# Optimization experiments

Hardware: AMD Instinct MI355X
Metric: run time of the kernel (lower is better)

The kernel has to match this reference:

```python
import jax, jax.numpy as jnp
import numpy as np

B, T, C, D = 8, 4096, 1024, 128  # batch, seq (=block_size), dim_embd, head_features

def setup_inputs() -> dict:
    key = jax.random.key(0)
    k1, k2, k3, k4 = jax.random.split(key, 4)
    s = 0.02
    return {
        "x": jax.random.normal(k1, (B, T, C), dtype=jnp.float32),
        "wq": jax.random.normal(k2, (C, D), dtype=jnp.float32) * s,
        "wk": jax.random.normal(k3, (C, D), dtype=jnp.float32) * s,
        "wv": jax.random.normal(k4, (C, D), dtype=jnp.float32) * s,
    }

def reference(x, wq, wk, wv):
    # q,k,v: [B,T,D]
    q = jnp.einsum('btc,cd->btd', x, wq)
    k = jnp.einsum('btc,cd->btd', x, wk)
    v = jnp.einsum('btc,cd->btd', x, wv)
    scale = k.shape[-1] ** -0.5
    wei = jnp.einsum('bqd,bkd->bqk', q, k) * scale  # [B,T,T]
    causal = jnp.tril(jnp.ones((T, T), dtype=bool))
    wei = jnp.where(causal, wei, -jnp.inf)
    attn = jax.nn.softmax(wei, axis=-1)  # dropout p=0.0 -> identity
    out = jnp.einsum('bqk,bkd->bqd', attn, v)  # [B,T,D]
    return out
```

## Files before the change

### kernel.cpp

```cpp
#include <hip/hip_runtime.h>

#define TT 4096
#define CC 1024
#define DD 128

typedef __attribute__((ext_vector_type(8))) short s16x8;
typedef __attribute__((ext_vector_type(4))) short s16x4;
typedef __attribute__((ext_vector_type(8))) __bf16 bf16x8;
typedef __attribute__((ext_vector_type(4))) float f32x4;

__device__ __forceinline__ short f2bf(float f) {
    union { float f; unsigned u; } v; v.f = f;
    unsigned r = v.u + 0x7fffu + ((v.u >> 16) & 1u);
    return (short)(r >> 16);
}

__device__ __forceinline__ unsigned cvt_pk(float lo, float hi) {
    unsigned r;
    asm("v_cvt_pk_bf16_f32 %0, %1, %2" : "=v"(r) : "v"(lo), "v"(hi));
    return r;
}

__device__ __forceinline__ f32x4 mfma16(s16x8 a, s16x8 b, f32x4 c) {
    return __builtin_amdgcn_mfma_f32_16x16x32_bf16(
        __builtin_bit_cast(bf16x8, a), __builtin_bit_cast(bf16x8, b), c, 0, 0, 0);
}

__device__ __forceinline__ void gload_lds16(const short* g, short* l) {
    __builtin_amdgcn_global_load_lds(
        (const __attribute__((address_space(1))) void*)g,
        (__attribute__((address_space(3))) void*)l, 16, 0, 0);
}

__global__ void wt_kernel(const float* __restrict__ wq, const float* __restrict__ wk,
                          const float* __restrict__ wv, short* __restrict__ wT) {
    int idx = blockIdx.x * 256 + threadIdx.x;
    int d = idx & 127;
    int c = (idx >> 7) & 1023;
    int wsel = idx >> 17;
    const float* w = (wsel == 0) ? wq : (wsel == 1) ? wk : wv;
    float v = w[(size_t)c * DD + d];
    if (wsel == 0) v *= 0.08838834764831845f;
    wT[(size_t)wsel * DD * CC + (size_t)d * CC + c] = f2bf(v);
}

__global__ __launch_bounds__(512)
void qkv_kernel(const float* __restrict__ x, const short* __restrict__ wT,
                short* __restrict__ qo, short* __restrict__ ko, short* __restrict__ vTo) {
    __shared__ short lw[2][384 * 64];
    const int mt = blockIdx.x;
    const int tid = threadIdx.x, lane = tid & 63, wid = tid >> 6;
    const int l15 = lane & 15, g = lane >> 4;
    const int wm = wid >> 1, wn = wid & 1;
    const int arow = mt * 128 + wm * 32 + l15;
    const float* xr0 = x + (size_t)arow * CC + g * 8;
    const float* xr1 = xr0 + (size_t)16 * CC;

    const f32x4 fz = {0.f, 0.f, 0.f, 0.f};
    f32x4 acc[2][12];
#pragma unroll
    for (int mr = 0; mr < 2; mr++)
#pragma unroll
        for (int nr = 0; nr < 12; nr++) acc[mr][nr] = fz;

    const int swr = wid * 48;
    const short* wsrc = wT + (size_t)(swr + (lane >> 3)) * CC + (lane & 7) * 8;

    float4 pa[2][2][2];
#define LOADA(kc) do { \
    _Pragma("unroll") for (int mr_ = 0; mr_ < 2; mr_++) \
    _Pragma("unroll") for (int ks_ = 0; ks_ < 2; ks_++) { \
        const float* p_ = (mr_ ? xr1 : xr0) + (kc) * 64 + ks_ * 32; \
        pa[mr_][ks_][0] = *(const float4*)p_; \
        pa[mr_][ks_][1] = *(const float4*)(p_ + 4); } \
} while (0)
#define STAGEW(kc, buf) do { \
    _Pragma("unroll") for (int j_ = 0; j_ < 6; j_++) \
        gload_lds16(wsrc + (size_t)(j_ * 8) * CC + (kc) * 64, &lw[buf][(swr + j_ * 8) * 64]); \
} while (0)

    LOADA(0);
    STAGEW(0, 0);
    asm volatile("s_waitcnt vmcnt(0)" ::: "memory");
    __builtin_amdgcn_s_barrier();
    int cur = 0;

    for (int kc = 0; kc < 16; kc++) {
        s16x8 af[2][2];
#pragma unroll
        for (int mr = 0; mr < 2; mr++)
#pragma unroll
            for (int ks = 0; ks < 2; ks++) {
                union { unsigned u[4]; s16x8 v; } cv;
                cv.u[0] = cvt_pk(pa[mr][ks][0].x, pa[mr][ks][0].y);
                cv.u[1] = cvt_pk(pa[mr][ks][0].z, pa[mr][ks][0].w);
                cv.u[2] = cvt_pk(pa[mr][ks][1].x, pa[mr][ks][1].y);
                cv.u[3] = cvt_pk(pa[mr][ks][1].z, pa[mr][ks][1].w);
                af[mr][ks] = cv.v;
            }
        if (kc < 15) { LOADA(kc + 1); STAGEW(kc + 1, cur ^ 1); }
        __builtin_amdgcn_s_setprio(1);
#pragma unroll
        for (int ks = 0; ks < 2; ks++)
#pragma unroll
            for (int nr = 0; nr < 12; nr++) {
                const s16x8 bfg = *(const s16x8*)
                    &lw[cur][(wn * 192 + nr * 16 + l15) * 64 + ks * 32 + g * 8];
                acc[0][nr] = mfma16(af[0][ks], bfg, acc[0][nr]);
                acc[1][nr] = mfma16(af[1][ks], bfg, acc[1][nr]);
            }
        __builtin_amdgcn_s_setprio(0);
        asm volatile("s_waitcnt vmcnt(0) lgkmcnt(0)" ::: "memory");
        __builtin_amdgcn_s_barrier();
        cur ^= 1;
    }

    const int bidx = mt >> 5;
    const int tb = (mt & 31) * 128 + wm * 32;
#pragma unroll
    for (int mr = 0; mr < 2; mr++)
#pragma unroll
        for (int nr = 0; nr < 12; nr++) {
            const int n = wn * 192 + nr * 16 + l15;
            if (n < 256) {
                short* dst; int d;
                if (n < 128) { dst = qo; d = n; } else { dst = ko; d = n - 128; }
#pragma unroll
                for (int i = 0; i < 4; i++) {
                    int t = tb + mr * 16 + g * 4 + i;
                    dst[((size_t)bidx * TT + t) * DD + d] = f2bf(acc[mr][nr][i]);
                }
            } else {
                const int d = n - 256;
                const int t = tb + mr * 16 + g * 4;
                uint2 u;
                u.x = cvt_pk(acc[mr][nr][0], acc[mr][nr][1]);
                u.y = cvt_pk(acc[mr][nr][2], acc[mr][nr][3]);
                *(uint2*)(vTo + ((size_t)bidx * DD + d) * TT + t) = u;
            }
        }
}

__device__ __forceinline__ void attn_stage(const short* kT, const short* vT, int kv0,
                                           short* lkb, short* lvb, int wid, int lane) {
#pragma unroll
    for (int j = 0; j < 4; j++) {
        int rbk = wid * 16 + j * 4;
        int rk = rbk + (lane >> 4);
        int ck = (lane & 15) ^ (rk & 7);
        gload_lds16(kT + (size_t)(kv0 + rk) * DD + ck * 8, lkb + rbk * 128);
        int rbv = wid * 32 + j * 8;
        int dv = rbv + (lane >> 3);
        int cv = (lane & 7) ^ (dv & 7);
        gload_lds16(vT + (size_t)dv * TT + kv0 + cv * 8, lvb + rbv * 64);
    }
}

__global__ __launch_bounds__(256)
void attn_kernel(const short* __restrict__ qb, const short* __restrict__ kb,
                 const short* __restrict__ vb, float* __restrict__ out,
                 float* __restrict__ opart, float2* __restrict__ mlpart) {
    const int qt = blockIdx.x;
    const int c  = blockIdx.y;
    const int b  = blockIdx.z;
    const int t0 = c * 16;
    if (t0 > qt) return;
    const int t1 = (t0 + 16 < qt + 1) ? t0 + 16 : qt + 1;
    const int nc = (qt >> 4) + 1;

    __shared__ short lk[2][64 * 128];
    __shared__ short lv[2][128 * 64];
    __shared__ short lp[4][1024];
    const int tid = threadIdx.x, lane = tid & 63, wid = tid >> 6;
    const int l15 = lane & 15, g = lane >> 4;
    const int wq0 = qt * 64 + wid * 16;
    const short* kT = kb + (size_t)b * TT * DD;
    const short* vT = vb + (size_t)b * DD * TT;
    char* lpw = (char*)&lp[wid][0];
    const f32x4 fz = {0.f, 0.f, 0.f, 0.f};

    s16x8 qf[4];
    {
        const short* qp = qb + ((size_t)b * TT + wq0 + l15) * DD + g * 8;
#pragma unroll
        for (int ks = 0; ks < 4; ks++) qf[ks] = *(const s16x8*)(qp + ks * 32);
    }
    f32x4 o[8];
#pragma unroll
    for (int n = 0; n < 8; n++) o[n] = fz;
    float rmax = -1e30f, rsum = 0.f;

    attn_stage(kT, vT, t0 * 64, lk[0], lv[0], wid, lane);
    asm volatile("s_waitcnt vmcnt(0)" ::: "memory");
    __builtin_amdgcn_s_barrier();
    int cur = 0;

    for (int t = t0; t < t1; t++) {
        if (t + 1 < t1) attn_stage(kT, vT, (t + 1) * 64, lk[cur ^ 1], lv[cur ^ 1], wid, lane);
        const int kv0 = t * 64;
        const char* lkc = (const char*)&lk[cur][0];
        const char* lvc = (const char*)&lv[cur][0];

        f32x4 s[4];
        __builtin_amdgcn_s_setprio(1);
#pragma unroll
        for (int sub = 0; sub < 4; sub++) {
            f32x4 a = fz;
#pragma unroll
            for (int ks = 0; ks < 4; ks++) {
                int row = sub * 16 + l15;
                int byte = (row * 256 + ks * 64 + g * 16) ^ ((row & 7) << 4);
                s16x8 kf = *(const s16x8*)(lkc + byte);
                a = mfma16(kf, qf[ks], a);
            }
            s[sub] = a;
        }
        __builtin_amdgcn_s_setprio(0);
        if (t == qt) {
#pragma unroll
            for (int sub = 0; sub < 4; sub++)
#pragma unroll
                for (int i = 0; i < 4; i++) {
                    int k = kv0 + sub * 16 + 4 * g + i;
                    if (k > wq0 + l15) s[sub][i] = -1e30f;
                }
        }
        float m0 = s[0][0];
#pragma unroll
        for (int sub = 0; sub < 4; sub++)
#pragma unroll
            for (int i = 0; i < 4; i++) m0 = fmaxf(m0, s[sub][i]);
        m0 = fmaxf(m0, __shfl_xor(m0, 16));
        m0 = fmaxf(m0, __shfl_xor(m0, 32));
        float mnew = fmaxf(rmax, m0);
        float scal = __expf(rmax - mnew);
        rmax = mnew;
        float ls = 0.f;
#pragma unroll
        for (int sub = 0; sub < 4; sub++)
#pragma unroll
            for (int i = 0; i < 4; i++) {
                float pv = __expf(s[sub][i] - mnew);
                s[sub][i] = pv;
                ls += pv;
            }
        ls += __shfl_xor(ls, 16);
        ls += __shfl_xor(ls, 32);
        rsum = rsum * scal + ls;
#pragma unroll
        for (int sub = 0; sub < 4; sub++) {
            uint2 w01;
            w01.x = cvt_pk(s[sub][0], s[sub][1]);
            w01.y = cvt_pk(s[sub][2], s[sub][3]);
            int byte = (l15 * 128 + sub * 32 + g * 8) ^ ((l15 & 7) << 4);
            *(uint2*)(lpw + byte) = w01;
        }
#pragma unroll
        for (int n = 0; n < 8; n++)
#pragma unroll
            for (int i = 0; i < 4; i++) o[n][i] *= scal;
        __builtin_amdgcn_s_setprio(1);
#pragma unroll
        for (int ks2 = 0; ks2 < 2; ks2++) {
            int pbyte = (l15 * 128 + ks2 * 64 + g * 16) ^ ((l15 & 7) << 4);
            s16x8 pf = *(const s16x8*)(lpw + pbyte);
#pragma unroll
            for (int n = 0; n < 8; n++) {
                int vrow = n * 16 + l15;
                int vbyte = (vrow * 128 + ks2 * 64 + g * 16) ^ ((vrow & 7) << 4);
                s16x8 vf = *(const s16x8*)(lvc + vbyte);
                o[n] = mfma16(vf, pf, o[n]);
            }
        }
        __builtin_amdgcn_s_setprio(0);
        asm volatile("s_waitcnt vmcnt(0) lgkmcnt(0)" ::: "memory");
        __builtin_amdgcn_s_barrier();
        cur ^= 1;
    }

    const int r = wid * 16 + l15;
    if (nc == 1) {
        float inv = 1.0f / rsum;
        float* orow = out + ((size_t)b * TT + qt * 64 + r) * DD;
#pragma unroll
        for (int n = 0; n < 8; n++) {
            float4 w;
            w.x = o[n][0] * inv; w.y = o[n][1] * inv;
            w.z = o[n][2] * inv; w.w = o[n][3] * inv;
            *(float4*)(orow + n * 16 + 4 * g) = w;
        }
    } else {
        const size_t pb = ((size_t)b * 48 + (qt - 16)) * 4 + c;
        float* prow = opart + pb * (64 * 128) + (size_t)r * 128;
#pragma unroll
        for (int n = 0; n < 8; n++) {
            float4 w;
            w.x = o[n][0]; w.y = o[n][1]; w.z = o[n][2]; w.w = o[n][3];
            *(float4*)(prow + n * 16 + 4 * g) = w;
        }
        if (g == 0) {
            float2 s2; s2.x = rmax; s2.y = rsum;
            mlpart[pb * 64 + r] = s2;
        }
    }
}

__global__ __launch_bounds__(256)
void comb_kernel(const float* __restrict__ opart, const float2* __restrict__ mlpart,
                 float* __restrict__ out) {
    const int qtm = blockIdx.x;
    const int b = blockIdx.y;
    const int qt = 16 + qtm;
    const int nc = (qt >> 4) + 1;
    const int tid = threadIdx.x;
    const int row = tid >> 2, quad = tid & 3;
    const size_t base = ((size_t)b * 48 + qtm) * 4;

    float M = -3e38f;
    for (int cc = 0; cc < nc; cc++)
        M = fmaxf(M, mlpart[(base + cc) * 64 + row].x);

    float acc[32];
#pragma unroll
    for (int k = 0; k < 32; k++) acc[k] = 0.f;
    float L = 0.f;
    for (int cc = 0; cc < nc; cc++) {
        float2 s = mlpart[(base + cc) * 64 + row];
        float wgt = __expf(s.x - M);
        L += wgt * s.y;
        const float* src = opart + (base + cc) * (64 * 128) + (size_t)row * 128 + quad * 32;
#pragma unroll
        for (int k = 0; k < 8; k++) {
            float4 v = *(const float4*)(src + k * 4);
            acc[k * 4 + 0] += wgt * v.x;
            acc[k * 4 + 1] += wgt * v.y;
            acc[k * 4 + 2] += wgt * v.z;
            acc[k * 4 + 3] += wgt * v.w;
        }
    }
    float inv = 1.0f / L;
    float* dst = out + ((size_t)b * TT + qt * 64 + row) * DD + quad * 32;
#pragma unroll
    for (int k = 0; k < 8; k++) {
        float4 w;
        w.x = acc[k * 4 + 0] * inv; w.y = acc[k * 4 + 1] * inv;
        w.z = acc[k * 4 + 2] * inv; w.w = acc[k * 4 + 3] * inv;
        *(float4*)(dst + k * 4) = w;
    }
}

extern "C" void kernel_launch(void* const* d_in, const int* in_sizes, int n_in,
                              void* d_out, int out_size, void* d_ws, size_t ws_size,
                              hipStream_t stream) {
    const float* x  = (const float*)d_in[0];
    const float* wq = (const float*)d_in[1];
    const float* wk = (const float*)d_in[2];
    const float* wv = (const float*)d_in[3];
    float* out = (float*)d_out;
    char* ws = (char*)d_ws;
    short* wT = (short*)ws;
    short* qb = (short*)(ws + 786432);
    short* kb = (short*)(ws + 786432 + 8388608);
    short* vb = (short*)(ws + 786432 + 16777216);
    float* opart = (float*)(ws + 786432 + 25165824);
    float2* mlpart = (float2*)(ws + 786432 + 25165824 + 50331648);

    wt_kernel<<<1536, 256, 0, stream>>>(wq, wk, wv, wT);
    qkv_kernel<<<256, 512, 0, stream>>>(x, wT, qb, kb, vb);
    attn_kernel<<<dim3(64, 4, 8), 256, 0, stream>>>(qb, kb, vb, out, opart, mlpart);
    comb_kernel<<<dim3(48, 8), 256, 0, stream>>>(opart, mlpart, out);
}
```

Before: 170.7 us.

## Use exp2 softmax with folded log2e, remap attention grid, nontemporal stores

Folds log2(e) into the Q weight scale so the softmax can use exp2f in place of __expf, in both the attention and combine kernels. Flattens the attention grid to 1D with batch as the fastest-varying index, which changes block scheduling order and the spread across CUs and caches. Switches output and partial-result writes, and the partial reads in the combine kernel, to nontemporal loads and stores to reduce cache pollution. Using exp2 directly may drop a multiply per element, but rounding the combined scale into bf16 changes numerics slightly.

```diff
diff --git a/kernel.cpp b/kernel.cpp
--- a/kernel.cpp
+++ b/kernel.cpp
@@ -8,6 +8,7 @@
 typedef __attribute__((ext_vector_type(4))) short s16x4;
 typedef __attribute__((ext_vector_type(8))) __bf16 bf16x8;
 typedef __attribute__((ext_vector_type(4))) float f32x4;
+typedef __attribute__((ext_vector_type(2))) float f32x2;
 
 __device__ __forceinline__ short f2bf(float f) {
     union { float f; unsigned u; } v; v.f = f;
@@ -40,7 +41,7 @@
     int wsel = idx >> 17;
     const float* w = (wsel == 0) ? wq : (wsel == 1) ? wk : wv;
     float v = w[(size_t)c * DD + d];
-    if (wsel == 0) v *= 0.08838834764831845f;
+    if (wsel == 0) v *= 0.08838834764831845f * 1.4426950408889634f;
     wT[(size_t)wsel * DD * CC + (size_t)d * CC + c] = f2bf(v);
 }
 
@@ -159,10 +160,12 @@
 __global__ __launch_bounds__(256)
 void attn_kernel(const short* __restrict__ qb, const short* __restrict__ kb,
                  const short* __restrict__ vb, float* __restrict__ out,
-                 float* __restrict__ opart, float2* __restrict__ mlpart) {
-    const int qt = blockIdx.x;
-    const int c  = blockIdx.y;
-    const int b  = blockIdx.z;
+                 float* __restrict__ opart, float* __restrict__ mlpart) {
+    const int id = blockIdx.x;
+    const int b  = id & 7;
+    const int r3 = id >> 3;
+    const int qt = r3 & 63;
+    const int c  = r3 >> 6;
     const int t0 = c * 16;
     if (t0 > qt) return;
     const int t1 = (t0 + 16 < qt + 1) ? t0 + 16 : qt + 1;
@@ -233,14 +236,14 @@
         m0 = fmaxf(m0, __shfl_xor(m0, 16));
         m0 = fmaxf(m0, __shfl_xor(m0, 32));
         float mnew = fmaxf(rmax, m0);
-        float scal = __expf(rmax - mnew);
+        float scal = exp2f(rmax - mnew);
         rmax = mnew;
         float ls = 0.f;
 #pragma unroll
         for (int sub = 0; sub < 4; sub++)
 #pragma unroll
             for (int i = 0; i < 4; i++) {
-                float pv = __expf(s[sub][i] - mnew);
+                float pv = exp2f(s[sub][i] - mnew);
                 s[sub][i] = pv;
                 ls += pv;
             }
@@ -284,29 +287,27 @@
         float* orow = out + ((size_t)b * TT + qt * 64 + r) * DD;
 #pragma unroll
         for (int n = 0; n < 8; n++) {
-            float4 w;
-            w.x = o[n][0] * inv; w.y = o[n][1] * inv;
-            w.z = o[n][2] * inv; w.w = o[n][3] * inv;
-            *(float4*)(orow + n * 16 + 4 * g) = w;
+            f32x4 w;
+            w[0] = o[n][0] * inv; w[1] = o[n][1] * inv;
+            w[2] = o[n][2] * inv; w[3] = o[n][3] * inv;
+            __builtin_nontemporal_store(w, (f32x4*)(orow + n * 16 + 4 * g));
         }
     } else {
         const size_t pb = ((size_t)b * 48 + (qt - 16)) * 4 + c;
         float* prow = opart + pb * (64 * 128) + (size_t)r * 128;
 #pragma unroll
         for (int n = 0; n < 8; n++) {
-            float4 w;
-            w.x = o[n][0]; w.y = o[n][1]; w.z = o[n][2]; w.w = o[n][3];
-            *(float4*)(prow + n * 16 + 4 * g) = w;
+            __builtin_nontemporal_store(o[n], (f32x4*)(prow + n * 16 + 4 * g));
         }
         if (g == 0) {
-            float2 s2; s2.x = rmax; s2.y = rsum;
-            mlpart[pb * 64 + r] = s2;
+            f32x2 s2; s2[0] = rmax; s2[1] = rsum;
+            __builtin_nontemporal_store(s2, (f32x2*)(mlpart + (pb * 64 + r) * 2));
         }
     }
 }
 
 __global__ __launch_bounds__(256)
-void comb_kernel(const float* __restrict__ opart, const float2* __restrict__ mlpart,
+void comb_kernel(const float* __restrict__ opart, const float* __restrict__ mlpart,
                  float* __restrict__ out) {
     const int qtm = blockIdx.x;
     const int b = blockIdx.y;
@@ -318,34 +319,35 @@
 
     float M = -3e38f;
     for (int cc = 0; cc < nc; cc++)
-        M = fmaxf(M, mlpart[(base + cc) * 64 + row].x);
+        M = fmaxf(M, mlpart[((base + cc) * 64 + row) * 2]);
 
     float acc[32];
 #pragma unroll
     for (int k = 0; k < 32; k++) acc[k] = 0.f;
     float L = 0.f;
     for (int cc = 0; cc < nc; cc++) {
-        float2 s = mlpart[(base + cc) * 64 + row];
-        float wgt = __expf(s.x - M);
-        L += wgt * s.y;
+        float sm = mlpart[((base + cc) * 64 + row) * 2];
+        float sl = mlpart[((base + cc) * 64 + row) * 2 + 1];
+        float wgt = exp2f(sm - M);
+        L += wgt * sl;
         const float* src = opart + (base + cc) * (64 * 128) + (size_t)row * 128 + quad * 32;
 #pragma unroll
         for (int k = 0; k < 8; k++) {
-            float4 v = *(const float4*)(src + k * 4);
-            acc[k * 4 + 0] += wgt * v.x;
-            acc[k * 4 + 1] += wgt * v.y;
-            acc[k * 4 + 2] += wgt * v.z;
-            acc[k * 4 + 3] += wgt * v.w;
+            f32x4 v = __builtin_nontemporal_load((const f32x4*)(src + k * 4));
+            acc[k * 4 + 0] += wgt * v[0];
+            acc[k * 4 + 1] += wgt * v[1];
+            acc[k * 4 + 2] += wgt * v[2];
+            acc[k * 4 + 3] += wgt * v[3];
         }
     }
     float inv = 1.0f / L;
     float* dst = out + ((size_t)b * TT + qt * 64 + row) * DD + quad * 32;
 #pragma unroll
     for (int k = 0; k < 8; k++) {
-        float4 w;
-        w.x = acc[k * 4 + 0] * inv; w.y = acc[k * 4 + 1] * inv;
-        w.z = acc[k * 4 + 2] * inv; w.w = acc[k * 4 + 3] * inv;
-        *(float4*)(dst + k * 4) = w;
+        f32x4 w;
+        w[0] = acc[k * 4 + 0] * inv; w[1] = acc[k * 4 + 1] * inv;
+        w[2] = acc[k * 4 + 2] * inv; w[3] = acc[k * 4 + 3] * inv;
+        __builtin_nontemporal_store(w, (f32x4*)(dst + k * 4));
     }
 }
 
@@ -363,10 +365,10 @@
     short* kb = (short*)(ws + 786432 + 8388608);
     short* vb = (short*)(ws + 786432 + 16777216);
     float* opart = (float*)(ws + 786432 + 25165824);
-    float2* mlpart = (float2*)(ws + 786432 + 25165824 + 50331648);
+    float* mlpart = (float*)(ws + 786432 + 25165824 + 50331648);
 
     wt_kernel<<<1536, 256, 0, stream>>>(wq, wk, wv, wT);
     qkv_kernel<<<256, 512, 0, stream>>>(x, wT, qb, kb, vb);
-    attn_kernel<<<dim3(64, 4, 8), 256, 0, stream>>>(qb, kb, vb, out, opart, mlpart);
+    attn_kernel<<<2048, 256, 0, stream>>>(qb, kb, vb, out, opart, mlpart);
     comb_kernel<<<dim3(48, 8), 256, 0, stream>>>(opart, mlpart, out);
 }
```

Measured after the change: 195.4 us. +14.5%, slower.
